# Optimization experiments

Hardware: AMD Instinct MI355X
Metric: run time of the kernel (lower is better)

## Reference

```python
import jax, jax.numpy as jnp
import numpy as np

D_MODEL = 1024
D_STATE = 8          # max(8, 16 // 2)
D_CONV = 4
D_INNER = int(1.5 * D_MODEL)   # expand = max(1.5, 2*0.75)
DT_RANK = (D_MODEL + 15) // 16 # 64
D_FF = 2 * D_MODEL
B, L = 2, 2048


def layer_norm(x, g, b, eps=1e-5):
    mu = jnp.mean(x, -1, keepdims=True)
    var = jnp.var(x, -1, keepdims=True)
    return (x - mu) * jax.lax.rsqrt(var + eps) * g + b


def setup_inputs() -> dict:
    key = jax.random.key(0)
    ks = jax.random.split(key, 12)
    def n(k, shape, scale=0.02):
        return jax.random.normal(k, shape, dtype=jnp.float32) * scale
    return {
        'x': jax.random.normal(ks[0], (B, L, D_MODEL), dtype=jnp.float32),
        'ln1_g': jnp.ones((D_MODEL,), jnp.float32),
        'ln1_b': jnp.zeros((D_MODEL,), jnp.float32),
        'ln2_g': jnp.ones((D_MODEL,), jnp.float32),
        'ln2_b': jnp.zeros((D_MODEL,), jnp.float32),
        'in_proj_w': n(ks[1], (2 * D_INNER, D_MODEL)),
        'conv_w': n(ks[2], (D_INNER, 1, D_CONV), 0.1),
        'conv_b': jnp.zeros((D_INNER,), jnp.float32),
        'x_proj_w': n(ks[3], (DT_RANK + 2 * D_STATE, D_INNER)),
        'dt_proj_w': n(ks[4], (D_INNER, DT_RANK), 0.1),
        'dt_proj_b': n(ks[5], (D_INNER,), 0.1),
        'A_log': jnp.log(jnp.broadcast_to(jnp.arange(1, D_STATE + 1, dtype=jnp.float32), (D_INNER, D_STATE))),
        'D': jnp.ones((D_INNER,), jnp.float32),
        'out_proj_w': n(ks[6], (D_MODEL, D_INNER)),
        'ffn_w1': n(ks[7], (D_FF, D_MODEL)),
        'ffn_b1': jnp.zeros((D_FF,), jnp.float32),
        'ffn_w2': n(ks[8], (D_MODEL, D_FF)),
        'ffn_b2': jnp.zeros((D_MODEL,), jnp.float32),
    }


def mamba(x, in_proj_w, conv_w, conv_b, x_proj_w, dt_proj_w, dt_proj_b, A_log, Dp, out_proj_w):
    # in_proj -> (x, z)
    xz = x @ in_proj_w.T                       # (B, L, 2*d_inner)
    xi, z = jnp.split(xz, 2, axis=-1)
    # depthwise causal conv over seq, kernel 4
    xc = jnp.transpose(xi, (0, 2, 1))          # (B, d_inner, L)
    xc = jax.lax.conv_general_dilated(
        xc, conv_w, window_strides=(1,), padding=[(D_CONV - 1, 0)],
        dimension_numbers=('NCH', 'OIH', 'NCH'), feature_group_count=D_INNER)
    xc = xc + conv_b[None, :, None]
    u = jax.nn.silu(jnp.transpose(xc, (0, 2, 1)))  # (B, L, d_inner)
    # x_proj -> dt, B, C
    x_dbl = u @ x_proj_w.T
    dt = x_dbl[..., :DT_RANK]
    Bm = x_dbl[..., DT_RANK:DT_RANK + D_STATE]
    Cm = x_dbl[..., DT_RANK + D_STATE:]
    delta = jax.nn.softplus(dt @ dt_proj_w.T + dt_proj_b)  # (B, L, d_inner)
    A = -jnp.exp(A_log)                                    # (d_inner, d_state)
    dA = jnp.exp(jnp.einsum('bld,dn->bldn', delta, A))     # (B, L, d_inner, d_state)
    dBu = jnp.einsum('bld,bln,bld->bldn', delta, Bm, u)
    # selective scan over time
    def step(h, inputs):
        dA_t, dBu_t, C_t = inputs
        h = dA_t * h + dBu_t                   # (B, d_inner, d_state)
        y = jnp.einsum('bdn,bn->bd', h, C_t)
        return h, y
    h0 = jnp.zeros((x.shape[0], D_INNER, D_STATE), x.dtype)
    _, ys = jax.lax.scan(step, h0, (jnp.moveaxis(dA, 1, 0), jnp.moveaxis(dBu, 1, 0), jnp.moveaxis(Cm, 1, 0)))
    y = jnp.moveaxis(ys, 0, 1) + u * Dp        # skip connection D*u
    y = y * jax.nn.silu(z)                     # gate
    return y @ out_proj_w.T


def reference(x, ln1_g, ln1_b, ln2_g, ln2_b, in_proj_w, conv_w, conv_b, x_proj_w,
              dt_proj_w, dt_proj_b, A_log, D, out_proj_w, ffn_w1, ffn_b1, ffn_w2, ffn_b2):
    residual = x
    xp = layer_norm(x, ln1_g, ln1_b)
    x = mamba(xp, in_proj_w, conv_w, conv_b, x_proj_w, dt_proj_w, dt_proj_b, A_log, D, out_proj_w) + residual
    xn = layer_norm(x, ln2_g, ln2_b)
    h = jax.nn.gelu(xn @ ffn_w1.T + ffn_b1, approximate=False)  # dropout is identity in eval
    return x + (h @ ffn_w2.T + ffn_b2)
```

## Files before the change

### kernel.cpp

```cpp
#include <hip/hip_runtime.h>
#include <math.h>

#define D_MODEL 1024
#define D_STATE 8
#define D_CONV  4
#define D_INNER 1536
#define DT_RANK 64
#define D_FF    2048
#define BATCH   2
#define SEQ     2048
#define NROWS   (BATCH*SEQ)
#define NC      32
#define LC      (SEQ/NC)
#define XPAD    128

typedef short bf16x8 __attribute__((ext_vector_type(8)));
typedef unsigned short u16x8 __attribute__((ext_vector_type(8)));
typedef float f32x4  __attribute__((ext_vector_type(4)));

__device__ inline unsigned short f2bf(float x) {
    union { float f; unsigned u; } v; v.f = x;
    unsigned r = v.u + 0x7fffu + ((v.u >> 16) & 1u);
    return (unsigned short)(r >> 16);
}
__device__ inline float bf2f(unsigned short h) {
    union { unsigned u; float f; } v; v.u = ((unsigned)h) << 16;
    return v.f;
}
__device__ inline float softplus_f(float x) {
    return (x > 20.0f) ? x : log1pf(__expf(x));
}
__device__ inline float gelu_f(float x) {
    return 0.5f * x * (1.0f + erff(x * 0.70710678118654752f));
}
__device__ inline float silu_f(float x) {
    return x / (1.0f + __expf(-x));
}
__device__ inline void gload16(const unsigned short* g, unsigned short* l) {
    typedef unsigned int u32;
    __builtin_amdgcn_global_load_lds(
        (const __attribute__((address_space(1))) u32*)g,
        (__attribute__((address_space(3))) u32*)l, 16, 0, 0);
}

__global__ __launch_bounds__(256) void wconv(const float* __restrict__ s0, unsigned short* __restrict__ d0,
                                             const float* __restrict__ s1, unsigned short* __restrict__ d1,
                                             const float* __restrict__ s2, unsigned short* __restrict__ d2,
                                             const float* __restrict__ s3, unsigned short* __restrict__ d3,
                                             const float* __restrict__ s4, unsigned short* __restrict__ d4) {
    int b = blockIdx.x;
    const float* s; unsigned short* d; int base;
    if      (b < 1536) { s = s0; d = d0; base = b * 2048; }
    else if (b < 1584) { s = s1; d = d1; base = (b - 1536) * 2048; }
    else if (b < 2352) { s = s2; d = d2; base = (b - 1584) * 2048; }
    else if (b < 3376) { s = s3; d = d3; base = (b - 2352) * 2048; }
    else               { s = s4; d = d4; base = (b - 3376) * 2048; }
    int i = base + threadIdx.x * 8;
    float4 v0 = *(const float4*)(s + i);
    float4 v1 = *(const float4*)(s + i + 4);
    ushort4 a, c;
    a.x = f2bf(v0.x); a.y = f2bf(v0.y); a.z = f2bf(v0.z); a.w = f2bf(v0.w);
    c.x = f2bf(v1.x); c.y = f2bf(v1.y); c.z = f2bf(v1.z); c.w = f2bf(v1.w);
    *(ushort4*)(d + i)     = a;
    *(ushort4*)(d + i + 4) = c;
}

__global__ __launch_bounds__(256) void xproj_pad(const float* __restrict__ src, unsigned short* __restrict__ dst) {
    int row = blockIdx.x;
    for (int c = threadIdx.x; c < D_INNER; c += 256)
        dst[row * D_INNER + c] = (row < 80) ? f2bf(src[row * D_INNER + c]) : (unsigned short)0;
}

__global__ __launch_bounds__(256) void ln_kernel(const float* __restrict__ x,
                                                 const float* __restrict__ g,
                                                 const float* __restrict__ b,
                                                 unsigned short* __restrict__ out) {
    __shared__ float sbuf[4];
    int row = blockIdx.x;
    int t = threadIdx.x;
    const float4* xr = (const float4*)(x + (size_t)row * D_MODEL);
    float4 v = xr[t];
    float s = v.x + v.y + v.z + v.w;
    for (int o = 32; o; o >>= 1) s += __shfl_down(s, o, 64);
    if ((t & 63) == 0) sbuf[t >> 6] = s;
    __syncthreads();
    float mu = (sbuf[0] + sbuf[1] + sbuf[2] + sbuf[3]) * (1.0f / D_MODEL);
    __syncthreads();
    float d0 = v.x - mu, d1 = v.y - mu, d2 = v.z - mu, d3 = v.w - mu;
    float q = d0*d0 + d1*d1 + d2*d2 + d3*d3;
    for (int o = 32; o; o >>= 1) q += __shfl_down(q, o, 64);
    if ((t & 63) == 0) sbuf[t >> 6] = q;
    __syncthreads();
    float var = (sbuf[0] + sbuf[1] + sbuf[2] + sbuf[3]) * (1.0f / D_MODEL);
    float rs = rsqrtf(var + 1e-5f);
    float4 gv = ((const float4*)g)[t];
    float4 bv = ((const float4*)b)[t];
    ushort4 st;
    st.x = f2bf(d0 * rs * gv.x + bv.x);
    st.y = f2bf(d1 * rs * gv.y + bv.y);
    st.z = f2bf(d2 * rs * gv.z + bv.z);
    st.w = f2bf(d3 * rs * gv.w + bv.w);
    ((ushort4*)(out + (size_t)row * D_MODEL))[t] = st;
}

#define EPI_F32        0
#define EPI_F32_BF16   1
#define EPI_SOFTPLUS   2
#define EPI_RESID      3
#define EPI_GELU_BF16  4
#define EPI_BIAS_RESID 5
#define EPI_BF16       6

template<int EPI, int SPLITK>
__global__ __launch_bounds__(256) void gemm_mfma(
    const unsigned short* __restrict__ A, int lda,
    const unsigned short* __restrict__ B, int ldb, int K,
    float* __restrict__ Cf, unsigned short* __restrict__ Cb, int ldc,
    const float* __restrict__ bias,
    const float* __restrict__ resid, int ldr) {
    __shared__ unsigned short As[3][128 * 32];
    __shared__ unsigned short Bs[3][128 * 32];
    int t = threadIdx.x, l = t & 63, w = t >> 6;
    int nx = gridDim.x;
    int nwg = nx * gridDim.y;
    int bid = blockIdx.y * nx + blockIdx.x;
    int q = nwg >> 3;
    int swz = (bid & 7) * q + (bid >> 3);
    int m0 = (swz / nx) * 128, n0 = (swz % nx) * 128;
    int kbase = (SPLITK > 1) ? blockIdx.z * K : 0;
    int c0 = 2 * w, c1 = 2 * w + 1;
    int srow = l >> 2, scol = (l & 3) * 8;
    const unsigned short* Ag0 = A + (size_t)(m0 + 16 * c0 + srow) * lda + kbase + scol;
    const unsigned short* Ag1 = A + (size_t)(m0 + 16 * c1 + srow) * lda + kbase + scol;
    const unsigned short* Bg0 = B + (size_t)(n0 + 16 * c0 + srow) * ldb + kbase + scol;
    const unsigned short* Bg1 = B + (size_t)(n0 + 16 * c1 + srow) * ldb + kbase + scol;
    int wr = w >> 1, wc = w & 1;
    int aoff = (wr * 64 + (l & 15)) * 32 + (l >> 4) * 8;
    int boff = (wc * 64 + (l & 15)) * 32 + (l >> 4) * 8;

    f32x4 acc[4][4] = {};
    int nt = K >> 5;

    {
        gload16(Ag0, &As[0][c0 * 512]);
        gload16(Ag1, &As[0][c1 * 512]);
        gload16(Bg0, &Bs[0][c0 * 512]);
        gload16(Bg1, &Bs[0][c1 * 512]);
        if (nt > 1) {
            gload16(Ag0 + 32, &As[1][c0 * 512]);
            gload16(Ag1 + 32, &As[1][c1 * 512]);
            gload16(Bg0 + 32, &Bs[1][c0 * 512]);
            gload16(Bg1 + 32, &Bs[1][c1 * 512]);
        }
    }

    int cur = 0;
    for (int ti = 0; ti < nt; ti++) {
        int pf = ti + 2;
        if (pf < nt) {
            int nb = cur - 1; if (nb < 0) nb += 3;
            int k0 = pf << 5;
            gload16(Ag0 + k0, &As[nb][c0 * 512]);
            gload16(Ag1 + k0, &As[nb][c1 * 512]);
            gload16(Bg0 + k0, &Bs[nb][c0 * 512]);
            gload16(Bg1 + k0, &Bs[nb][c1 * 512]);
        }
        int rem = nt - 1 - ti;
        if (rem >= 2)      asm volatile("s_waitcnt vmcnt(8)" ::: "memory");
        else if (rem == 1) asm volatile("s_waitcnt vmcnt(4)" ::: "memory");
        else               asm volatile("s_waitcnt vmcnt(0)" ::: "memory");
        __builtin_amdgcn_s_barrier();

        const unsigned short* Ab = &As[cur][0];
        const unsigned short* Bb = &Bs[cur][0];
        bf16x8 af[4], bfv[4];
        #pragma unroll
        for (int i = 0; i < 4; i++) af[i] = *(const bf16x8*)(Ab + aoff + i * 512);
        #pragma unroll
        for (int i = 0; i < 4; i++) bfv[i] = *(const bf16x8*)(Bb + boff + i * 512);
        __builtin_amdgcn_s_setprio(1);
        #pragma unroll
        for (int mi = 0; mi < 4; mi++)
            #pragma unroll
            for (int ni = 0; ni < 4; ni++)
                acc[mi][ni] = __builtin_amdgcn_mfma_f32_16x16x32_bf16(af[mi], bfv[ni], acc[mi][ni], 0, 0, 0);
        __builtin_amdgcn_s_setprio(0);
        __builtin_amdgcn_s_barrier();
        cur++; if (cur == 3) cur = 0;
    }

    if (SPLITK > 1) Cf += (size_t)blockIdx.z * NROWS * ldc;
    int colb = n0 + wc * 64 + (l & 15);
    int rowb = m0 + wr * 64 + (l >> 4) * 4;
    #pragma unroll
    for (int ni = 0; ni < 4; ni++) {
        int col = colb + ni * 16;
        float bv = 0.0f;
        if (EPI == EPI_SOFTPLUS || EPI == EPI_GELU_BF16 || EPI == EPI_BIAS_RESID) bv = bias[col];
        #pragma unroll
        for (int mi = 0; mi < 4; mi++) {
            #pragma unroll
            for (int j = 0; j < 4; j++) {
                int row = rowb + mi * 16 + j;
                float v = acc[mi][ni][j];
                if (EPI == EPI_SOFTPLUS)        v = softplus_f(v + bv);
                else if (EPI == EPI_GELU_BF16)  v = gelu_f(v + bv);
                else if (EPI == EPI_RESID)      v = v + resid[(size_t)row * ldr + col];
                else if (EPI == EPI_BIAS_RESID) v = v + bv + resid[(size_t)row * ldr + col];
                if (EPI == EPI_GELU_BF16 || EPI == EPI_BF16) {
                    Cb[(size_t)row * ldc + col] = f2bf(v);
                } else {
                    Cf[(size_t)row * ldc + col] = v;
                    if (EPI == EPI_F32_BF16) Cb[(size_t)row * ldc + col] = f2bf(v);
                }
            }
        }
    }
}

__global__ __launch_bounds__(256) void xdbl_reduce(const float* __restrict__ part,
                                                   float* __restrict__ xdbl,
                                                   unsigned short* __restrict__ xdbl_bf) {
    int i = blockIdx.x * 256 + threadIdx.x;
    const size_t seg = (size_t)NROWS * XPAD;
    float s = part[i] + part[i + seg] + part[i + 2 * seg] + part[i + 3 * seg];
    xdbl[i] = s;
    xdbl_bf[i] = f2bf(s);
}

__global__ __launch_bounds__(256) void conv_silu(const unsigned short* __restrict__ xz,
                                                 const float* __restrict__ w,
                                                 const float* __restrict__ cb,
                                                 unsigned short* __restrict__ u) {
    int idx = (blockIdx.x * 256 + threadIdx.x) * 8;
    int d = idx % D_INNER;
    int bl = idx / D_INNER;
    int l = bl & (SEQ - 1);
    float acc[8];
    float4 wv[8];
    #pragma unroll
    for (int j = 0; j < 8; j++) wv[j] = *(const float4*)(w + (d + j) * 4);
    float4 cb0 = *(const float4*)(cb + d);
    float4 cb1 = *(const float4*)(cb + d + 4);
    acc[0] = cb0.x; acc[1] = cb0.y; acc[2] = cb0.z; acc[3] = cb0.w;
    acc[4] = cb1.x; acc[5] = cb1.y; acc[6] = cb1.z; acc[7] = cb1.w;
    #pragma unroll
    for (int k = 0; k < 4; k++) {
        int lp = l - 3 + k;
        if (lp >= 0) {
            u16x8 s = *(const u16x8*)(xz + (size_t)(bl - 3 + k) * (2 * D_INNER) + d);
            #pragma unroll
            for (int j = 0; j < 8; j++) {
                float wk = (k == 0) ? wv[j].x : (k == 1) ? wv[j].y : (k == 2) ? wv[j].z : wv[j].w;
                acc[j] += bf2f((unsigned short)s[j]) * wk;
            }
        }
    }
    u16x8 o;
    #pragma unroll
    for (int j = 0; j < 8; j++) o[j] = f2bf(silu_f(acc[j]));
    *(u16x8*)(u + idx) = o;
}

__global__ __launch_bounds__(256) void scan_passA(const float* __restrict__ delta,
                                                  const unsigned short* __restrict__ u,
                                                  const float* __restrict__ xdbl,
                                                  const float* __restrict__ A_log,
                                                  float* __restrict__ P,
                                                  float* __restrict__ S) {
    int d = blockIdx.x * 256 + threadIdx.x;
    int c = blockIdx.y, b = blockIdx.z;
    __shared__ float bc[LC][16];
    int base_row = b * SEQ + c * LC;
    for (int e = threadIdx.x; e < LC * 16; e += 256) {
        int lrr = e >> 4, col = e & 15;
        bc[lrr][col] = xdbl[(size_t)(base_row + lrr) * XPAD + DT_RANK + col];
    }
    __syncthreads();
    float Ad[8];
    #pragma unroll
    for (int n = 0; n < 8; n++) Ad[n] = -__expf(A_log[d * 8 + n]);
    float prod[8], hs[8];
    #pragma unroll
    for (int n = 0; n < 8; n++) { prod[n] = 1.0f; hs[n] = 0.0f; }
    for (int lrr = 0; lrr < LC; lrr++) {
        int row = base_row + lrr;
        float dl = delta[(size_t)row * D_INNER + d];
        float uu = bf2f(u[(size_t)row * D_INNER + d]);
        float du = dl * uu;
        #pragma unroll
        for (int n = 0; n < 8; n++) {
            float dA = __expf(dl * Ad[n]);
            prod[n] *= dA;
            hs[n] = dA * hs[n] + du * bc[lrr][n];
        }
    }
    size_t o = ((size_t)((size_t)b * NC + c) * D_INNER + d) * 8;
    #pragma unroll
    for (int n = 0; n < 8; n++) { P[o + n] = prod[n]; S[o + n] = hs[n]; }
}

__global__ __launch_bounds__(256) void scan_passB(const float* __restrict__ P,
                                                  const float* __restrict__ S,
                                                  float* __restrict__ hstart) {
    int tid = blockIdx.x * 256 + threadIdx.x;
    int b = tid / (D_INNER * 8);
    int rem = tid % (D_INNER * 8);
    float h = 0.0f;
    for (int c = 0; c < NC; c++) {
        size_t o = (size_t)(b * NC + c) * (D_INNER * 8) + rem;
        hstart[o] = h;
        h = P[o] * h + S[o];
    }
}

__global__ __launch_bounds__(256) void scan_passC(const float* __restrict__ delta,
                                                  const unsigned short* __restrict__ u,
                                                  const float* __restrict__ xdbl,
                                                  const float* __restrict__ A_log,
                                                  const float* __restrict__ hstart,
                                                  const unsigned short* __restrict__ xz,
                                                  const float* __restrict__ Dp,
                                                  unsigned short* __restrict__ ygate) {
    int d = blockIdx.x * 256 + threadIdx.x;
    int c = blockIdx.y, b = blockIdx.z;
    __shared__ float bc[LC][16];
    int base_row = b * SEQ + c * LC;
    for (int e = threadIdx.x; e < LC * 16; e += 256) {
        int lrr = e >> 4, col = e & 15;
        bc[lrr][col] = xdbl[(size_t)(base_row + lrr) * XPAD + DT_RANK + col];
    }
    __syncthreads();
    float Ad[8];
    #pragma unroll
    for (int n = 0; n < 8; n++) Ad[n] = -__expf(A_log[d * 8 + n]);
    float h[8];
    size_t ho = ((size_t)((size_t)b * NC + c) * D_INNER + d) * 8;
    #pragma unroll
    for (int n = 0; n < 8; n++) h[n] = hstart[ho + n];
    float Dd = Dp[d];
    for (int lrr = 0; lrr < LC; lrr++) {
        int row = base_row + lrr;
        float dl = delta[(size_t)row * D_INNER + d];
        float uu = bf2f(u[(size_t)row * D_INNER + d]);
        float du = dl * uu;
        float y = 0.0f;
        #pragma unroll
        for (int n = 0; n < 8; n++) {
            float dA = __expf(dl * Ad[n]);
            h[n] = dA * h[n] + du * bc[lrr][n];
            y += h[n] * bc[lrr][8 + n];
        }
        y += uu * Dd;
        float z = bf2f(xz[(size_t)row * (2 * D_INNER) + D_INNER + d]);
        ygate[(size_t)row * D_INNER + d] = f2bf(y * silu_f(z));
    }
}

extern "C" void kernel_launch(void* const* d_in, const int* in_sizes, int n_in,
                              void* d_out, int out_size, void* d_ws, size_t ws_size,
                              hipStream_t stream) {
    const float* x         = (const float*)d_in[0];
    const float* ln1_g     = (const float*)d_in[1];
    const float* ln1_b     = (const float*)d_in[2];
    const float* ln2_g     = (const float*)d_in[3];
    const float* ln2_b     = (const float*)d_in[4];
    const float* in_proj_w = (const float*)d_in[5];
    const float* conv_w    = (const float*)d_in[6];
    const float* conv_b    = (const float*)d_in[7];
    const float* x_proj_w  = (const float*)d_in[8];
    const float* dt_proj_w = (const float*)d_in[9];
    const float* dt_proj_b = (const float*)d_in[10];
    const float* A_log     = (const float*)d_in[11];
    const float* Dp        = (const float*)d_in[12];
    const float* out_proj_w= (const float*)d_in[13];
    const float* ffn_w1    = (const float*)d_in[14];
    const float* ffn_b1    = (const float*)d_in[15];
    const float* ffn_w2    = (const float*)d_in[16];
    const float* ffn_b2    = (const float*)d_in[17];
    float* out = (float*)d_out;

    float* xdbl  = (float*)d_ws;
    float* delta = xdbl + (size_t)NROWS * XPAD;
    float* P     = delta + (size_t)NROWS * D_INNER;
    float* S     = P + (size_t)BATCH * NC * D_INNER * 8;
    float* hst   = S + (size_t)BATCH * NC * D_INNER * 8;
    float* x2    = hst + (size_t)BATCH * NC * D_INNER * 8;
    float* part  = x2;
    unsigned short* xz_bf   = (unsigned short*)(x2 + (size_t)NROWS * D_MODEL);
    unsigned short* xp_bf   = xz_bf + (size_t)NROWS * 2 * D_INNER;
    unsigned short* u_bf    = xp_bf + (size_t)NROWS * D_MODEL;
    unsigned short* xdbl_bf = u_bf + (size_t)NROWS * D_INNER;
    unsigned short* yg_bf   = xdbl_bf + (size_t)NROWS * XPAD;
    unsigned short* w_in    = yg_bf + (size_t)NROWS * D_INNER;
    unsigned short* w_xp    = w_in + (size_t)2 * D_INNER * D_MODEL;
    unsigned short* w_dt    = w_xp + (size_t)XPAD * D_INNER;
    unsigned short* w_out   = w_dt + (size_t)D_INNER * DT_RANK;
    unsigned short* w_f1    = w_out + (size_t)D_MODEL * D_INNER;
    unsigned short* w_f2    = w_f1 + (size_t)D_FF * D_MODEL;
    unsigned short* hff_bf  = xz_bf;

    wconv<<<4400, 256, 0, stream>>>(in_proj_w, w_in, dt_proj_w, w_dt, out_proj_w, w_out,
                                    ffn_w1, w_f1, ffn_w2, w_f2);
    xproj_pad<<<XPAD, 256, 0, stream>>>(x_proj_w, w_xp);
    ln_kernel<<<NROWS, 256, 0, stream>>>(x, ln1_g, ln1_b, xp_bf);
    gemm_mfma<EPI_BF16, 1><<<dim3(3072 / 128, NROWS / 128), 256, 0, stream>>>(
        xp_bf, D_MODEL, w_in, D_MODEL, D_MODEL, nullptr, xz_bf, 2 * D_INNER, nullptr, nullptr, 0);
    conv_silu<<<(NROWS * D_INNER) / (256 * 8), 256, 0, stream>>>(xz_bf, conv_w, conv_b, u_bf);
    gemm_mfma<EPI_F32, 4><<<dim3(1, NROWS / 128, 4), 256, 0, stream>>>(
        u_bf, D_INNER, w_xp, D_INNER, D_INNER / 4, part, nullptr, XPAD, nullptr, nullptr, 0);
    xdbl_reduce<<<(NROWS * XPAD) / 256, 256, 0, stream>>>(part, xdbl, xdbl_bf);
    gemm_mfma<EPI_SOFTPLUS, 1><<<dim3(D_INNER / 128, NROWS / 128), 256, 0, stream>>>(
        xdbl_bf, XPAD, w_dt, DT_RANK, DT_RANK, delta, nullptr, D_INNER, dt_proj_b, nullptr, 0);
    scan_passA<<<dim3(D_INNER / 256, NC, BATCH), 256, 0, stream>>>(delta, u_bf, xdbl, A_log, P, S);
    scan_passB<<<(BATCH * D_INNER * 8) / 256, 256, 0, stream>>>(P, S, hst);
    scan_passC<<<dim3(D_INNER / 256, NC, BATCH), 256, 0, stream>>>(delta, u_bf, xdbl, A_log, hst, xz_bf, Dp, yg_bf);
    gemm_mfma<EPI_RESID, 1><<<dim3(D_MODEL / 128, NROWS / 128), 256, 0, stream>>>(
        yg_bf, D_INNER, w_out, D_INNER, D_INNER, x2, nullptr, D_MODEL, nullptr, x, D_MODEL);
    ln_kernel<<<NROWS, 256, 0, stream>>>(x2, ln2_g, ln2_b, xp_bf);
    gemm_mfma<EPI_GELU_BF16, 1><<<dim3(D_FF / 128, NROWS / 128), 256, 0, stream>>>(
        xp_bf, D_MODEL, w_f1, D_MODEL, D_MODEL, nullptr, hff_bf, D_FF, ffn_b1, nullptr, 0);
    gemm_mfma<EPI_BIAS_RESID, 1><<<dim3(D_MODEL / 128, NROWS / 128), 256, 0, stream>>>(
        hff_bf, D_FF, w_f2, D_FF, D_FF, out, nullptr, D_MODEL, ffn_b2, x2, D_MODEL);
}
```

Measured before the change: 313.3 us.

## Add 8-wave 256-row GEMM with swizzled LDS and phased ping-pong schedule

Adds a new 512-thread GEMM kernel with 256xBN tiles, XOR-swizzled LDS layout, double-buffered K=64 stages and explicit barrier-phased MFMA/load interleaving with setprio. It replaces the four large projection GEMMs (in_proj, out_proj, FFN1, FFN2). The aim is more data reuse per tile and better overlap of global loads with MFMA work. In exchange, grids have fewer workgroups, which can reduce occupancy on the smaller GEMMs (e.g. out_proj and FFN2 with 128 blocks). The heavy barrier use could also stall if the phases are unbalanced.

New measurement: 306.2 us. -2.3%, faster.

```diff
diff --git a/kernel.cpp b/kernel.cpp
--- a/kernel.cpp
+++ b/kernel.cpp
@@ -42,6 +42,11 @@
         (const __attribute__((address_space(1))) u32*)g,
         (__attribute__((address_space(3))) u32*)l, 16, 0, 0);
 }
+
+#define PHASE_SYNC_PRE()  do { __builtin_amdgcn_s_barrier(); __builtin_amdgcn_sched_barrier(0); \
+                               asm volatile("s_waitcnt lgkmcnt(0)" ::: "memory"); \
+                               __builtin_amdgcn_sched_barrier(0); } while (0)
+#define PHASE_SYNC_POST() do { __builtin_amdgcn_s_barrier(); __builtin_amdgcn_sched_barrier(0); } while (0)
 
 __global__ __launch_bounds__(256) void wconv(const float* __restrict__ s0, unsigned short* __restrict__ d0,
                                              const float* __restrict__ s1, unsigned short* __restrict__ d1,
@@ -111,6 +116,170 @@
 #define EPI_BIAS_RESID 5
 #define EPI_BF16       6
 
+template<int WN, int EPI>
+__global__ __launch_bounds__(512, 2) void gemm8p(
+    const unsigned short* __restrict__ A, int lda,
+    const unsigned short* __restrict__ Bm, int ldb, int K,
+    float* __restrict__ Cf, unsigned short* __restrict__ Cb, int ldc,
+    const float* __restrict__ bias,
+    const float* __restrict__ resid, int ldr) {
+    constexpr int WM = 8 / WN;
+    constexpr int BN = WN * 64;
+    constexpr int RW = 256 / WM;
+    constexpr int CW = 64;
+    constexpr int MI = RW / 16;
+    constexpr int NI = CW / 16;
+    constexpr int MIH = MI / 2, NIH = NI / 2;
+    constexpr int ABYTES = 256 * 128;
+    constexpr int BBYTES = BN * 128;
+    constexpr int BOFF = 2 * ABYTES;
+    __shared__ unsigned short lds[(2 * ABYTES + 2 * BBYTES) / 2];
+
+    const int t = threadIdx.x, l = t & 63, w = t >> 6;
+    const int wr = w / WN, wc = w % WN;
+
+    const int nx = gridDim.x;
+    const int nwg = nx * gridDim.y;
+    int bid = blockIdx.y * nx + blockIdx.x;
+    int q = nwg >> 3;
+    int swz = (bid & 7) * q + (bid >> 3);
+    const int m0 = (swz / nx) * 256, n0 = (swz % nx) * BN;
+
+    const int sr = l >> 3;
+    const int sj = ((l & 7) * 16) ^ (((l >> 5) & 1) << 5);
+    const int row_l = w * 8;
+    const int row_c = (w >> 2) * 64 + (w & 3) * 8;
+
+    auto STG = [&](int bufbyte, int rowbase, const unsigned short* G, int ldg, int gbase, int kt) {
+        unsigned short* dst = (unsigned short*)((char*)lds + bufbyte + rowbase * 128);
+        const unsigned short* src = G + (size_t)(gbase + rowbase + sr) * ldg + kt * 64 + (sj >> 1);
+        gload16(src, dst);
+    };
+    auto S_Ah0 = [&](int b, int kt) {
+        if (WN == 4) { STG(b * ABYTES, row_l, A, lda, m0, kt);       STG(b * ABYTES, 128 + row_l, A, lda, m0, kt); }
+        else         { STG(b * ABYTES, row_c, A, lda, m0, kt);       STG(b * ABYTES, 128 + row_c, A, lda, m0, kt); }
+    };
+    auto S_Ah1 = [&](int b, int kt) {
+        if (WN == 4) { STG(b * ABYTES, 64 + row_l, A, lda, m0, kt);  STG(b * ABYTES, 192 + row_l, A, lda, m0, kt); }
+        else         { STG(b * ABYTES, 32 + row_c, A, lda, m0, kt);  STG(b * ABYTES, 160 + row_c, A, lda, m0, kt); }
+    };
+    auto S_Bc0 = [&](int b, int kt) {
+        if (WN == 4) { STG(BOFF + b * BBYTES, row_c, Bm, ldb, n0, kt); STG(BOFF + b * BBYTES, 128 + row_c, Bm, ldb, n0, kt); }
+        else         { STG(BOFF + b * BBYTES, row_c, Bm, ldb, n0, kt); }
+    };
+    auto S_Bc1 = [&](int b, int kt) {
+        if (WN == 4) { STG(BOFF + b * BBYTES, 32 + row_c, Bm, ldb, n0, kt); STG(BOFF + b * BBYTES, 160 + row_c, Bm, ldb, n0, kt); }
+        else         { STG(BOFF + b * BBYTES, 32 + row_c, Bm, ldb, n0, kt); }
+    };
+
+    auto LD = [&](int bytebase, int row, int kb) -> bf16x8 {
+        int o = bytebase + row * 128 + (kb ^ (((row >> 2) & 1) << 5));
+        return *(const bf16x8*)((const char*)lds + o);
+    };
+
+    f32x4 acc[MI][NI] = {};
+    bf16x8 af[MIH][2], b0v[NIH][2], b1v[NIH][2];
+
+    auto LDA_set = [&](int buf, int qr, auto& dst) {
+        #pragma unroll
+        for (int mi = 0; mi < MIH; mi++)
+            #pragma unroll
+            for (int ks = 0; ks < 2; ks++)
+                dst[mi][ks] = LD(buf * ABYTES, wr * RW + qr * (RW / 2) + mi * 16 + (l & 15),
+                                 ks * 64 + (l >> 4) * 16);
+    };
+    auto LDB_set = [&](int buf, int qc, auto& dst) {
+        #pragma unroll
+        for (int ni2 = 0; ni2 < NIH; ni2++)
+            #pragma unroll
+            for (int ks = 0; ks < 2; ks++)
+                dst[ni2][ks] = LD(BOFF + buf * BBYTES, wc * CW + qc * 32 + ni2 * 16 + (l & 15),
+                                  ks * 64 + (l >> 4) * 16);
+    };
+    auto MFMA_Q = [&](int qr, int qc, auto& a_, auto& b_) {
+        __builtin_amdgcn_s_setprio(1);
+        #pragma unroll
+        for (int mi = 0; mi < MIH; mi++)
+            #pragma unroll
+            for (int ni2 = 0; ni2 < NIH; ni2++)
+                #pragma unroll
+                for (int ks = 0; ks < 2; ks++)
+                    acc[qr * MIH + mi][qc * NIH + ni2] =
+                        __builtin_amdgcn_mfma_f32_16x16x32_bf16(a_[mi][ks], b_[ni2][ks],
+                                                                acc[qr * MIH + mi][qc * NIH + ni2], 0, 0, 0);
+        __builtin_amdgcn_s_setprio(0);
+    };
+    auto VMW = [&](bool last) {
+        if (last)            asm volatile("s_waitcnt vmcnt(0)" ::: "memory");
+        else if (WN == 4)    asm volatile("s_waitcnt vmcnt(6)" ::: "memory");
+        else                 asm volatile("s_waitcnt vmcnt(5)" ::: "memory");
+        __builtin_amdgcn_sched_barrier(0);
+    };
+
+    const int ni_ = K >> 7;
+
+    S_Ah0(0, 0); S_Ah1(0, 0); S_Bc0(0, 0); S_Bc1(0, 0);
+    S_Ah0(1, 1); S_Ah1(1, 1); S_Bc0(1, 1); S_Bc1(1, 1);
+    if (WN == 4) asm volatile("s_waitcnt vmcnt(8)" ::: "memory");
+    else         asm volatile("s_waitcnt vmcnt(6)" ::: "memory");
+    __builtin_amdgcn_s_barrier();
+    __builtin_amdgcn_sched_barrier(0);
+
+    for (int i = 0; i < ni_; i++) {
+        const bool last = (i == ni_ - 1);
+        const int t2 = 2 * i + 2, t3 = 2 * i + 3;
+        LDA_set(0, 0, af); LDB_set(0, 0, b0v);
+        if (i) S_Bc0(1, 2 * i + 1);
+        PHASE_SYNC_PRE(); MFMA_Q(0, 0, af, b0v); PHASE_SYNC_POST();
+        LDB_set(0, 1, b1v);
+        if (!last) S_Ah0(0, t2);
+        PHASE_SYNC_PRE(); MFMA_Q(0, 1, af, b1v); PHASE_SYNC_POST();
+        LDA_set(0, 1, af);
+        PHASE_SYNC_PRE(); MFMA_Q(1, 1, af, b1v); PHASE_SYNC_POST();
+        LDB_set(0, 0, b0v);
+        if (!last) { S_Ah1(0, t2); S_Bc1(0, t2); }
+        VMW(last);
+        PHASE_SYNC_PRE(); MFMA_Q(1, 0, af, b0v); PHASE_SYNC_POST();
+        LDA_set(1, 0, af); LDB_set(1, 0, b0v);
+        if (!last) S_Bc0(0, t2);
+        PHASE_SYNC_PRE(); MFMA_Q(0, 0, af, b0v); PHASE_SYNC_POST();
+        LDB_set(1, 1, b1v);
+        if (!last) S_Ah0(1, t3);
+        PHASE_SYNC_PRE(); MFMA_Q(0, 1, af, b1v); PHASE_SYNC_POST();
+        LDA_set(1, 1, af);
+        PHASE_SYNC_PRE(); MFMA_Q(1, 1, af, b1v); PHASE_SYNC_POST();
+        LDB_set(1, 0, b0v);
+        if (!last) { S_Ah1(1, t3); S_Bc1(1, t3); }
+        VMW(last);
+        PHASE_SYNC_PRE(); MFMA_Q(1, 0, af, b0v); PHASE_SYNC_POST();
+    }
+
+    #pragma unroll
+    for (int ni2 = 0; ni2 < NI; ni2++) {
+        int col = n0 + wc * CW + ni2 * 16 + (l & 15);
+        float bv = 0.0f;
+        if (EPI == EPI_SOFTPLUS || EPI == EPI_GELU_BF16 || EPI == EPI_BIAS_RESID) bv = bias[col];
+        #pragma unroll
+        for (int mi = 0; mi < MI; mi++) {
+            #pragma unroll
+            for (int j = 0; j < 4; j++) {
+                int row = m0 + wr * RW + mi * 16 + (l >> 4) * 4 + j;
+                float v = acc[mi][ni2][j];
+                if (EPI == EPI_SOFTPLUS)        v = softplus_f(v + bv);
+                else if (EPI == EPI_GELU_BF16)  v = gelu_f(v + bv);
+                else if (EPI == EPI_RESID)      v = v + resid[(size_t)row * ldr + col];
+                else if (EPI == EPI_BIAS_RESID) v = v + bv + resid[(size_t)row * ldr + col];
+                if (EPI == EPI_GELU_BF16 || EPI == EPI_BF16) {
+                    Cb[(size_t)row * ldc + col] = f2bf(v);
+                } else {
+                    Cf[(size_t)row * ldc + col] = v;
+                    if (EPI == EPI_F32_BF16) Cb[(size_t)row * ldc + col] = f2bf(v);
+                }
+            }
+        }
+    }
+}
+
 template<int EPI, int SPLITK>
 __global__ __launch_bounds__(256) void gemm_mfma(
     const unsigned short* __restrict__ A, int lda,
@@ -141,17 +310,15 @@
     f32x4 acc[4][4] = {};
     int nt = K >> 5;
 
-    {
-        gload16(Ag0, &As[0][c0 * 512]);
-        gload16(Ag1, &As[0][c1 * 512]);
-        gload16(Bg0, &Bs[0][c0 * 512]);
-        gload16(Bg1, &Bs[0][c1 * 512]);
-        if (nt > 1) {
-            gload16(Ag0 + 32, &As[1][c0 * 512]);
-            gload16(Ag1 + 32, &As[1][c1 * 512]);
-            gload16(Bg0 + 32, &Bs[1][c0 * 512]);
-            gload16(Bg1 + 32, &Bs[1][c1 * 512]);
-        }
+    gload16(Ag0, &As[0][c0 * 512]);
+    gload16(Ag1, &As[0][c1 * 512]);
+    gload16(Bg0, &Bs[0][c0 * 512]);
+    gload16(Bg1, &Bs[0][c1 * 512]);
+    if (nt > 1) {
+        gload16(Ag0 + 32, &As[1][c0 * 512]);
+        gload16(Ag1 + 32, &As[1][c1 * 512]);
+        gload16(Bg0 + 32, &Bs[1][c0 * 512]);
+        gload16(Bg1 + 32, &Bs[1][c1 * 512]);
     }
 
     int cur = 0;
@@ -404,7 +571,7 @@
                                     ffn_w1, w_f1, ffn_w2, w_f2);
     xproj_pad<<<XPAD, 256, 0, stream>>>(x_proj_w, w_xp);
     ln_kernel<<<NROWS, 256, 0, stream>>>(x, ln1_g, ln1_b, xp_bf);
-    gemm_mfma<EPI_BF16, 1><<<dim3(3072 / 128, NROWS / 128), 256, 0, stream>>>(
+    gemm8p<4, EPI_BF16><<<dim3(3072 / 256, NROWS / 256), 512, 0, stream>>>(
         xp_bf, D_MODEL, w_in, D_MODEL, D_MODEL, nullptr, xz_bf, 2 * D_INNER, nullptr, nullptr, 0);
     conv_silu<<<(NROWS * D_INNER) / (256 * 8), 256, 0, stream>>>(xz_bf, conv_w, conv_b, u_bf);
     gemm_mfma<EPI_F32, 4><<<dim3(1, NROWS / 128, 4), 256, 0, stream>>>(
@@ -415,11 +582,11 @@
     scan_passA<<<dim3(D_INNER / 256, NC, BATCH), 256, 0, stream>>>(delta, u_bf, xdbl, A_log, P, S);
     scan_passB<<<(BATCH * D_INNER * 8) / 256, 256, 0, stream>>>(P, S, hst);
     scan_passC<<<dim3(D_INNER / 256, NC, BATCH), 256, 0, stream>>>(delta, u_bf, xdbl, A_log, hst, xz_bf, Dp, yg_bf);
-    gemm_mfma<EPI_RESID, 1><<<dim3(D_MODEL / 128, NROWS / 128), 256, 0, stream>>>(
+    gemm8p<2, EPI_RESID><<<dim3(D_MODEL / 128, NROWS / 256), 512, 0, stream>>>(
         yg_bf, D_INNER, w_out, D_INNER, D_INNER, x2, nullptr, D_MODEL, nullptr, x, D_MODEL);
     ln_kernel<<<NROWS, 256, 0, stream>>>(x2, ln2_g, ln2_b, xp_bf);
-    gemm_mfma<EPI_GELU_BF16, 1><<<dim3(D_FF / 128, NROWS / 128), 256, 0, stream>>>(
+    gemm8p<2, EPI_GELU_BF16><<<dim3(D_FF / 128, NROWS / 256), 512, 0, stream>>>(
         xp_bf, D_MODEL, w_f1, D_MODEL, D_MODEL, nullptr, hff_bf, D_FF, ffn_b1, nullptr, 0);
-    gemm_mfma<EPI_BIAS_RESID, 1><<<dim3(D_MODEL / 128, NROWS / 128), 256, 0, stream>>>(
+    gemm8p<2, EPI_BIAS_RESID><<<dim3(D_MODEL / 128, NROWS / 256), 512, 0, stream>>>(
         hff_bf, D_FF, w_f2, D_FF, D_FF, out, nullptr, D_MODEL, ffn_b2, x2, D_MODEL);
 }
```
